# Optimization experiments

Hardware: AMD Instinct MI355X
Metric: run time of the kernel (lower is better)

Reference implementation:

```python
import jax, jax.numpy as jnp
import numpy as np

T, H, I, E, K = 2048, 1024, 768, 32, 4  # tokens, hidden, expert intermediate, n_experts, top_k


def setup_inputs() -> dict:
    key = jax.random.key(0)
    k0, k1, k2, k3, k4 = jax.random.split(key, 5)
    scale = 0.02
    return {
        "x": jax.random.normal(k0, (T, H), dtype=jnp.float32),
        "gate_w": jax.random.normal(k1, (E, H), dtype=jnp.float32) * scale,   # router linear [E, H]
        "w_gate": jax.random.normal(k2, (E, I, H), dtype=jnp.float32) * scale,  # gate_proj per expert
        "w_up": jax.random.normal(k3, (E, I, H), dtype=jnp.float32) * scale,    # up_proj per expert
        "w_down": jax.random.normal(k4, (E, H, I), dtype=jnp.float32) * scale,  # down_proj per expert
    }


def reference(x, gate_w, w_gate, w_up, w_down):
    # Router: dense gate linear + softmax + top-k + renormalize
    logits = x @ gate_w.T                              # [T, E]
    probs = jax.nn.softmax(logits, axis=-1)
    top_w, top_i = jax.lax.top_k(probs, K)             # [T, K]
    top_w = top_w / jnp.sum(top_w, axis=-1, keepdims=True)  # renormalize=True
    # Dense combine weights [T, E] (zero for unselected experts)
    tok = jnp.arange(T, dtype=jnp.int32)[:, None]
    combine = jnp.zeros((T, E), dtype=x.dtype).at[tok, top_i].add(top_w)

    # Scan over experts: each expert is a SwiGLU MLP; masked-dense combine.
    def step(acc, ws):
        w1, w3, w2, ce = ws                            # [I,H], [I,H], [H,I], [T]
        h = (jax.nn.silu(x @ w1.T) * (x @ w3.T)) @ w2.T  # [T, H]
        return acc + ce[:, None] * h, None

    out, _ = jax.lax.scan(step, jnp.zeros_like(x), (w_gate, w_up, w_down, combine.T))
    return out
```

## Files before the change

kernel.cpp:

```cpp
#include <hip/hip_runtime.h>
#include <hip/hip_bf16.h>
#include <stdint.h>

#define T_TOK 2048
#define HDIM  1024
#define IDIM  768
#define NEXP  32
#define TOPK  4
#define NPAIR (T_TOK*TOPK)
#define MTILE 384
#define MAXMT 64

typedef __attribute__((ext_vector_type(8))) short bf16x8;
typedef __attribute__((ext_vector_type(4))) float f32x4;

#define SBAR0() __builtin_amdgcn_sched_barrier(0)
#define LBAR()  do{ asm volatile("s_waitcnt lgkmcnt(0)" ::: "memory"); \
                    __builtin_amdgcn_s_barrier(); SBAR0(); }while(0)

__device__ __forceinline__ unsigned short f2bf(float f){
  union { float f; unsigned u; } v; v.f = f;
  unsigned r = (v.u + 0x7fffu + ((v.u >> 16) & 1u)) >> 16;
  return (unsigned short)r;
}

__device__ __forceinline__ unsigned pack_bf2(float lo, float hi){
  __hip_bfloat162 h2 = __float22bfloat162_rn(float2{lo, hi});
  union { __hip_bfloat162 h; unsigned u; } v; v.h = h2;
  return v.u;
}

__global__ __launch_bounds__(256) void k_convert_x(const float* __restrict__ x,
                                                   ushort* __restrict__ xb){
  int idx = blockIdx.x*256 + threadIdx.x;
  float4 v = ((const float4*)x)[idx];
  ushort4 o; o.x=f2bf(v.x); o.y=f2bf(v.y); o.z=f2bf(v.z); o.w=f2bf(v.w);
  ((ushort4*)xb)[idx] = o;
}

__global__ __launch_bounds__(256) void k_router(const float* __restrict__ x,
                                                const float* __restrict__ gw,
                                                int* __restrict__ ei, float* __restrict__ wv,
                                                int* __restrict__ counts){
  int wid  = threadIdx.x >> 6;
  int lane = threadIdx.x & 63;
  int t = blockIdx.x*4 + wid;
  float xv[16];
  #pragma unroll
  for (int i=0;i<16;i++) xv[i] = x[t*HDIM + i*64 + lane];
  float p[NEXP];
  #pragma unroll
  for (int e=0;e<NEXP;e++){
    const float* w = gw + e*HDIM;
    float a = 0.f;
    #pragma unroll
    for (int i=0;i<16;i++) a = fmaf(xv[i], w[i*64+lane], a);
    #pragma unroll
    for (int off=32; off>=1; off>>=1) a += __shfl_xor(a, off, 64);
    p[e] = a;
  }
  float m = p[0];
  #pragma unroll
  for (int e=1;e<NEXP;e++) m = fmaxf(m, p[e]);
  #pragma unroll
  for (int e=0;e<NEXP;e++) p[e] = __expf(p[e]-m);
  unsigned used = 0; int sel[TOPK]; float sw[TOPK]; float wsum = 0.f;
  #pragma unroll
  for (int k=0;k<TOPK;k++){
    float best = -1.f; int bi = 0;
    #pragma unroll
    for (int e=0;e<NEXP;e++){
      bool ok = (((used>>e)&1u)==0u) && (p[e] > best);
      best = ok ? p[e] : best; bi = ok ? e : bi;
    }
    used |= 1u<<bi; sel[k]=bi; sw[k]=best; wsum += best;
  }
  if (lane==0){
    float inv = 1.f/wsum;
    #pragma unroll
    for (int k=0;k<TOPK;k++){
      ei[t*TOPK+k] = sel[k];
      wv[t*TOPK+k] = sw[k]*inv;
      atomicAdd(&counts[sel[k]], 1);
    }
  }
}

__global__ void k_offsets(const int* __restrict__ counts, int* __restrict__ offsets,
                          int* __restrict__ mtE, int* __restrict__ mtM0,
                          int* __restrict__ nmt){
  if (threadIdx.x==0 && blockIdx.x==0){
    int s=0;
    for (int e=0;e<NEXP;e++){ offsets[e]=s; s+=counts[e]; }
    offsets[NEXP]=s;
    int nm=0;
    for (int e=0;e<NEXP;e++){
      int ne = counts[e];
      for (int m0=0; m0<ne && nm<MAXMT; m0+=MTILE){ mtE[nm]=e; mtM0[nm]=m0; nm++; }
    }
    nmt[0]=nm;
  }
}

__global__ __launch_bounds__(256) void k_scatter(const int* __restrict__ ei,
                                                 const int* __restrict__ offsets,
                                                 int* __restrict__ cursor,
                                                 int* __restrict__ slot_tk,
                                                 int* __restrict__ tk_slot){
  int g = blockIdx.x*256 + threadIdx.x;
  int e = ei[g];
  int pos = atomicAdd(&cursor[e], 1);
  int slot = offsets[e] + pos;
  slot_tk[slot] = g;
  tk_slot[g] = slot;
}

__global__ __launch_bounds__(512,3) void k_gateup(const ushort* __restrict__ xb,
    const float* __restrict__ w1, const float* __restrict__ w3,
    const int* __restrict__ offsets, const int* __restrict__ slot_tk,
    const int* __restrict__ mtE, const int* __restrict__ mtM0, const int* __restrict__ nmt,
    ushort* __restrict__ act){
  const int NH = 8;
  int bi  = blockIdx.x;
  int xcd = bi & 7, j = bi >> 3;
  int mti = (j/24)*8 + xcd;
  int it  = j % 24;
  if (mti >= nmt[0]) return;
  int e    = mtE[mti];
  int m0   = mtM0[mti];
  int off0 = offsets[e];
  int ne   = offsets[e+1]-off0;
  int ibase = it*32;

  __shared__ ushort Bls[2][64][136];
  __shared__ int toks[MTILE];

  int tid = threadIdx.x, wid = tid>>6, lane = tid&63;
  if (tid < MTILE){
    int slot = off0 + m0 + tid;
    int fb = slot_tk[off0] >> 2;
    toks[tid] = (m0 + tid < ne) ? (slot_tk[slot] >> 2) : fb;
  }
  __syncthreads();

  const float* bp[4]; int brow_s[4];
  #pragma unroll
  for (int s=0;s<4;s++){
    int row = s*16 + wid*2 + (lane>>5);
    brow_s[s] = row;
    int mat = row>>5, ir = row&31;
    bp[s] = (mat ? w3 : w1) + (size_t)e*IDIM*HDIM
          + (size_t)(ibase+ir)*HDIM + (lane&31)*4;
  }
  int q = lane>>4;
  const ushort* arow[3];
  #pragma unroll
  for (int m=0;m<3;m++){
    int row = wid*48 + m*16 + (lane&15);
    arow[m] = xb + (size_t)toks[row]*HDIM + q*8;
  }

  f32x4 accg[3][2], accu[3][2];
  #pragma unroll
  for (int m=0;m<3;m++)
    #pragma unroll
    for (int n=0;n<2;n++){ accg[m][n]=(f32x4){0,0,0,0}; accu[m][n]=(f32x4){0,0,0,0}; }

  float4 breg[4];
  bf16x8 aA[3][4];

  auto loadB = [&](int t){
    #pragma unroll
    for (int s=0;s<4;s++) breg[s] = *(const float4*)(bp[s] + t*128);
  };
  auto writeB = [&](int buf){
    #pragma unroll
    for (int s=0;s<4;s++){
      uint2 u; u.x = pack_bf2(breg[s].x, breg[s].y); u.y = pack_bf2(breg[s].z, breg[s].w);
      *(uint2*)(&Bls[buf][brow_s[s]][(lane&31)*4]) = u;
    }
  };
  auto loadA = [&](int t){
    #pragma unroll
    for (int m=0;m<3;m++)
      #pragma unroll
      for (int kk=0;kk<4;kk++)
        aA[m][kk] = *(const bf16x8*)(arow[m] + t*128 + kk*32);
  };
  auto compute = [&](int buf){
    #pragma unroll
    for (int kk=0;kk<4;kk++){
      #pragma unroll
      for (int nf=0;nf<2;nf++){
        bf16x8 bg = *(const bf16x8*)(&Bls[buf][     nf*16 + (lane&15)][kk*32 + q*8]);
        bf16x8 bu = *(const bf16x8*)(&Bls[buf][32 + nf*16 + (lane&15)][kk*32 + q*8]);
        #pragma unroll
        for (int m=0;m<3;m++){
          accg[m][nf] = __builtin_amdgcn_mfma_f32_16x16x32_bf16(aA[m][kk], bg, accg[m][nf], 0,0,0);
          accu[m][nf] = __builtin_amdgcn_mfma_f32_16x16x32_bf16(aA[m][kk], bu, accu[m][nf], 0,0,0);
        }
      }
    }
  };

  loadB(0);
  writeB(0);
  loadA(0);
  SBAR0();
  loadB(1);
  LBAR();

  #pragma unroll 2
  for (int h=0; h<NH; ++h){
    compute(h&1);
    if (h+1 < NH){
      writeB((h+1)&1);
      loadA(h+1);
      SBAR0();
      if (h+2 < NH) loadB(h+2);
      LBAR();
    }
  }

  int nval = ne - m0; if (nval > MTILE) nval = MTILE;
  #pragma unroll
  for (int m=0;m<3;m++)
    #pragma unroll
    for (int nf=0;nf<2;nf++)
      #pragma unroll
      for (int r=0;r<4;r++){
        int row = wid*48 + m*16 + (lane>>4)*4 + r;
        if (row < nval){
          float g = accg[m][nf][r], u = accu[m][nf][r];
          float sval = g / (1.f + __expf(-g)) * u;
          act[(size_t)(off0+m0+row)*IDIM + ibase + nf*16 + (lane&15)] = f2bf(sval);
        }
      }
}

__global__ __launch_bounds__(512,3) void k_down(const ushort* __restrict__ act,
    const float* __restrict__ w2, const int* __restrict__ offsets,
    const int* __restrict__ mtE, const int* __restrict__ mtM0, const int* __restrict__ nmt,
    float* __restrict__ pout){
  const int NH = 6;
  int bi  = blockIdx.x;
  int xcd = bi & 7, j = bi >> 3;
  int mti = (j>>4)*8 + xcd;
  int ht  = j & 15;
  if (mti >= nmt[0]) return;
  int e    = mtE[mti];
  int m0   = mtM0[mti];
  int off0 = offsets[e], ne = offsets[e+1]-off0;
  int hbase = ht*64;

  __shared__ ushort Bls[2][64][136];

  int tid = threadIdx.x, wid = tid>>6, lane = tid&63;

  const float* bp[4]; int brow_s[4];
  #pragma unroll
  for (int s=0;s<4;s++){
    int row = s*16 + wid*2 + (lane>>5);
    brow_s[s] = row;
    bp[s] = w2 + (size_t)e*HDIM*IDIM + (size_t)(hbase+row)*IDIM + (lane&31)*4;
  }
  int q = lane>>4;
  const ushort* arow[3];
  #pragma unroll
  for (int m=0;m<3;m++){
    int row = m0 + wid*48 + m*16 + (lane&15);
    row = (row < ne) ? row : (ne-1);
    arow[m] = act + (size_t)(off0+row)*IDIM + q*8;
  }

  f32x4 acc[3][4];
  #pragma unroll
  for (int m=0;m<3;m++)
    #pragma unroll
    for (int n=0;n<4;n++) acc[m][n]=(f32x4){0,0,0,0};

  float4 breg[4];
  bf16x8 aA[3][4];

  auto loadB = [&](int t){
    #pragma unroll
    for (int s=0;s<4;s++) breg[s] = *(const float4*)(bp[s] + t*128);
  };
  auto writeB = [&](int buf){
    #pragma unroll
    for (int s=0;s<4;s++){
      uint2 u; u.x = pack_bf2(breg[s].x, breg[s].y); u.y = pack_bf2(breg[s].z, breg[s].w);
      *(uint2*)(&Bls[buf][brow_s[s]][(lane&31)*4]) = u;
    }
  };
  auto loadA = [&](int t){
    #pragma unroll
    for (int m=0;m<3;m++)
      #pragma unroll
      for (int kk=0;kk<4;kk++)
        aA[m][kk] = *(const bf16x8*)(arow[m] + t*128 + kk*32);
  };
  auto compute = [&](int buf){
    #pragma unroll
    for (int kk=0;kk<4;kk++){
      #pragma unroll
      for (int nf=0;nf<4;nf++){
        bf16x8 bw = *(const bf16x8*)(&Bls[buf][nf*16 + (lane&15)][kk*32 + q*8]);
        #pragma unroll
        for (int m=0;m<3;m++)
          acc[m][nf] = __builtin_amdgcn_mfma_f32_16x16x32_bf16(aA[m][kk], bw, acc[m][nf], 0,0,0);
      }
    }
  };

  loadB(0);
  writeB(0);
  loadA(0);
  SBAR0();
  loadB(1);
  LBAR();

  #pragma unroll 2
  for (int h=0; h<NH; ++h){
    compute(h&1);
    if (h+1 < NH){
      writeB((h+1)&1);
      loadA(h+1);
      SBAR0();
      if (h+2 < NH) loadB(h+2);
      LBAR();
    }
  }

  int nval = ne - m0; if (nval > MTILE) nval = MTILE;
  #pragma unroll
  for (int m=0;m<3;m++)
    #pragma unroll
    for (int nf=0;nf<4;nf++)
      #pragma unroll
      for (int r=0;r<4;r++){
        int row = wid*48 + m*16 + (lane>>4)*4 + r;
        if (row < nval)
          pout[(size_t)(off0+m0+row)*HDIM + hbase + nf*16 + (lane&15)] = acc[m][nf][r];
      }
}

__global__ __launch_bounds__(256) void k_combine(const float* __restrict__ pout,
    const int* __restrict__ tk_slot, const float* __restrict__ wv,
    float* __restrict__ out){
  int t = blockIdx.x;
  int c = threadIdx.x;
  float a0=0,a1=0,a2=0,a3=0;
  #pragma unroll
  for (int k=0;k<TOPK;k++){
    int slot = tk_slot[t*TOPK+k];
    float w  = wv[t*TOPK+k];
    float4 v = *(const float4*)(pout + (size_t)slot*HDIM + c*4);
    a0 = fmaf(w, v.x, a0); a1 = fmaf(w, v.y, a1);
    a2 = fmaf(w, v.z, a2); a3 = fmaf(w, v.w, a3);
  }
  float4 o; o.x=a0; o.y=a1; o.z=a2; o.w=a3;
  *(float4*)(out + (size_t)t*HDIM + c*4) = o;
}

extern "C" void kernel_launch(void* const* d_in, const int* in_sizes, int n_in,
                              void* d_out, int out_size, void* d_ws, size_t ws_size,
                              hipStream_t stream){
  const float* x  = (const float*)d_in[0];
  const float* gw = (const float*)d_in[1];
  const float* w1 = (const float*)d_in[2];
  const float* w3 = (const float*)d_in[3];
  const float* w2 = (const float*)d_in[4];
  float* out = (float*)d_out;

  char* ws = (char*)d_ws;
  size_t off = 0;
  ushort* xb   = (ushort*)(ws + off); off += (size_t)T_TOK*HDIM*2;
  ushort* act  = (ushort*)(ws + off); off += (size_t)NPAIR*IDIM*2;
  float*  pout = (float*) (ws + off); off += (size_t)NPAIR*HDIM*4;
  int* counts  = (int*)(ws + off); off += NEXP*4;
  int* cursor  = (int*)(ws + off); off += NEXP*4;
  int* offsets = (int*)(ws + off); off += (NEXP+1)*4;
  int* mtE     = (int*)(ws + off); off += MAXMT*4;
  int* mtM0    = (int*)(ws + off); off += MAXMT*4;
  int* nmt     = (int*)(ws + off); off += 4;
  off = (off + 255) & ~(size_t)255;
  int*   ei      = (int*)  (ws + off); off += (size_t)NPAIR*4;
  float* wvp     = (float*)(ws + off); off += (size_t)NPAIR*4;
  int*   slot_tk = (int*)  (ws + off); off += (size_t)NPAIR*4;
  int*   tk_slot = (int*)  (ws + off); off += (size_t)NPAIR*4;

  hipMemsetAsync(counts, 0, 2*NEXP*4, stream);

  k_convert_x<<<T_TOK*HDIM/1024, 256, 0, stream>>>(x, xb);
  k_router<<<T_TOK/4, 256, 0, stream>>>(x, gw, ei, wvp, counts);
  k_offsets<<<1, 64, 0, stream>>>(counts, offsets, mtE, mtM0, nmt);
  k_scatter<<<NPAIR/256, 256, 0, stream>>>(ei, offsets, cursor, slot_tk, tk_slot);
  k_gateup<<<1536, 512, 0, stream>>>(xb, w1, w3, offsets, slot_tk, mtE, mtM0, nmt, act);
  k_down<<<1024, 512, 0, stream>>>(act, w2, offsets, mtE, mtM0, nmt, pout);
  k_combine<<<T_TOK, 256, 0, stream>>>(pout, tk_slot, wvp, out);
}
```

Before: 238.0 us.

## Triple-buffer GEMM K-loop with smaller K-steps and fuse x conversion into router

The gate/up and down GEMM kernels move from a double-buffered 128-wide K step to a triple-buffered 64-wide K step. Weights are prefetched three stages ahead in registers and the loop is fully unrolled, and launch bounds rise to allow four blocks per CU. Separately, the fp32-to-bf16 conversion of x is folded into the router kernel, which removes one kernel launch and one extra read pass over x. The trade-off is more barriers per unit of work and higher register pressure under the tighter occupancy bound.

New measurement: 223.2 us. -6.2%, faster.

```diff
diff --git a/kernel.cpp b/kernel.cpp
--- a/kernel.cpp
+++ b/kernel.cpp
@@ -30,18 +30,11 @@
   return v.u;
 }
 
-__global__ __launch_bounds__(256) void k_convert_x(const float* __restrict__ x,
-                                                   ushort* __restrict__ xb){
-  int idx = blockIdx.x*256 + threadIdx.x;
-  float4 v = ((const float4*)x)[idx];
-  ushort4 o; o.x=f2bf(v.x); o.y=f2bf(v.y); o.z=f2bf(v.z); o.w=f2bf(v.w);
-  ((ushort4*)xb)[idx] = o;
-}
-
 __global__ __launch_bounds__(256) void k_router(const float* __restrict__ x,
                                                 const float* __restrict__ gw,
                                                 int* __restrict__ ei, float* __restrict__ wv,
-                                                int* __restrict__ counts){
+                                                int* __restrict__ counts,
+                                                ushort* __restrict__ xb){
   int wid  = threadIdx.x >> 6;
   int lane = threadIdx.x & 63;
   int t = blockIdx.x*4 + wid;
@@ -83,6 +76,12 @@
       wv[t*TOPK+k] = sw[k]*inv;
       atomicAdd(&counts[sel[k]], 1);
     }
+  }
+  #pragma unroll
+  for (int kq=0;kq<4;kq++){
+    float4 v = *(const float4*)(x + (size_t)t*HDIM + (kq*64+lane)*4);
+    ushort4 o; o.x=f2bf(v.x); o.y=f2bf(v.y); o.z=f2bf(v.z); o.w=f2bf(v.w);
+    *(ushort4*)(xb + (size_t)t*HDIM + (kq*64+lane)*4) = o;
   }
 }
 
@@ -115,16 +114,16 @@
   tk_slot[g] = slot;
 }
 
-__global__ __launch_bounds__(512,3) void k_gateup(const ushort* __restrict__ xb,
+__global__ __launch_bounds__(512,4) void k_gateup(const ushort* __restrict__ xb,
     const float* __restrict__ w1, const float* __restrict__ w3,
     const int* __restrict__ offsets, const int* __restrict__ slot_tk,
     const int* __restrict__ mtE, const int* __restrict__ mtM0, const int* __restrict__ nmt,
     ushort* __restrict__ act){
-  const int NH = 8;
+  const int NHS = 16;
   int bi  = blockIdx.x;
-  int xcd = bi & 7, j = bi >> 3;
-  int mti = (j/24)*8 + xcd;
-  int it  = j % 24;
+  int s   = bi >> 3;
+  int mti = (s/24)*8 + (bi&7);
+  int it  = s % 24;
   if (mti >= nmt[0]) return;
   int e    = mtE[mti];
   int m0   = mtM0[mti];
@@ -132,7 +131,7 @@
   int ne   = offsets[e+1]-off0;
   int ibase = it*32;
 
-  __shared__ ushort Bls[2][64][136];
+  __shared__ ushort Bls[3][64][72];
   __shared__ int toks[MTILE];
 
   int tid = threadIdx.x, wid = tid>>6, lane = tid&63;
@@ -143,14 +142,14 @@
   }
   __syncthreads();
 
-  const float* bp[4]; int brow_s[4];
-  #pragma unroll
-  for (int s=0;s<4;s++){
-    int row = s*16 + wid*2 + (lane>>5);
-    brow_s[s] = row;
+  const float* bp[2]; int brow_s[2];
+  #pragma unroll
+  for (int ss=0;ss<2;ss++){
+    int row = ss*32 + wid*4 + (lane>>4);
+    brow_s[ss] = row;
     int mat = row>>5, ir = row&31;
-    bp[s] = (mat ? w3 : w1) + (size_t)e*IDIM*HDIM
-          + (size_t)(ibase+ir)*HDIM + (lane&31)*4;
+    bp[ss] = (mat ? w3 : w1) + (size_t)e*IDIM*HDIM
+           + (size_t)(ibase+ir)*HDIM + (lane&15)*4;
   }
   int q = lane>>4;
   const ushort* arow[3];
@@ -166,30 +165,30 @@
     #pragma unroll
     for (int n=0;n<2;n++){ accg[m][n]=(f32x4){0,0,0,0}; accu[m][n]=(f32x4){0,0,0,0}; }
 
-  float4 breg[4];
-  bf16x8 aA[3][4];
-
-  auto loadB = [&](int t){
-    #pragma unroll
-    for (int s=0;s<4;s++) breg[s] = *(const float4*)(bp[s] + t*128);
-  };
-  auto writeB = [&](int buf){
-    #pragma unroll
-    for (int s=0;s<4;s++){
-      uint2 u; u.x = pack_bf2(breg[s].x, breg[s].y); u.y = pack_bf2(breg[s].z, breg[s].w);
-      *(uint2*)(&Bls[buf][brow_s[s]][(lane&31)*4]) = u;
+  float4 b0[2], b1[2], b2[2];
+  bf16x8 aA[3][2];
+
+  auto loadB = [&](int t, float4 (&d)[2]){
+    d[0] = *(const float4*)(bp[0] + t*64);
+    d[1] = *(const float4*)(bp[1] + t*64);
+  };
+  auto writeB = [&](int buf, const float4 (&sv)[2]){
+    #pragma unroll
+    for (int ss=0;ss<2;ss++){
+      uint2 u; u.x = pack_bf2(sv[ss].x, sv[ss].y); u.y = pack_bf2(sv[ss].z, sv[ss].w);
+      *(uint2*)(&Bls[buf][brow_s[ss]][(lane&15)*4]) = u;
     }
   };
   auto loadA = [&](int t){
     #pragma unroll
     for (int m=0;m<3;m++)
       #pragma unroll
-      for (int kk=0;kk<4;kk++)
-        aA[m][kk] = *(const bf16x8*)(arow[m] + t*128 + kk*32);
-  };
-  auto compute = [&](int buf){
-    #pragma unroll
-    for (int kk=0;kk<4;kk++){
+      for (int kk=0;kk<2;kk++)
+        aA[m][kk] = *(const bf16x8*)(arow[m] + t*64 + kk*32);
+  };
+  auto computeK = [&](int buf){
+    #pragma unroll
+    for (int kk=0;kk<2;kk++){
       #pragma unroll
       for (int nf=0;nf<2;nf++){
         bf16x8 bg = *(const bf16x8*)(&Bls[buf][     nf*16 + (lane&15)][kk*32 + q*8]);
@@ -203,24 +202,27 @@
     }
   };
 
-  loadB(0);
-  writeB(0);
+  loadB(0, b0);
   loadA(0);
-  SBAR0();
-  loadB(1);
+  loadB(1, b1);
+  writeB(0, b0);
+  loadB(2, b2);
   LBAR();
 
-  #pragma unroll 2
-  for (int h=0; h<NH; ++h){
-    compute(h&1);
-    if (h+1 < NH){
-      writeB((h+1)&1);
-      loadA(h+1);
-      SBAR0();
-      if (h+2 < NH) loadB(h+2);
-      LBAR();
-    }
-  }
+#define GUSTEP(h, cb, wb, BW, BL) \
+  computeK(cb); \
+  if ((h)+1 < NHS) loadA((h)+1); \
+  if ((h)+3 < NHS) loadB((h)+3, BL); \
+  if ((h)+1 < NHS) writeB(wb, BW); \
+  LBAR();
+
+  GUSTEP(0, 0, 1, b1, b0)  GUSTEP(1, 1, 2, b2, b1)  GUSTEP(2, 2, 0, b0, b2)
+  GUSTEP(3, 0, 1, b1, b0)  GUSTEP(4, 1, 2, b2, b1)  GUSTEP(5, 2, 0, b0, b2)
+  GUSTEP(6, 0, 1, b1, b0)  GUSTEP(7, 1, 2, b2, b1)  GUSTEP(8, 2, 0, b0, b2)
+  GUSTEP(9, 0, 1, b1, b0)  GUSTEP(10,1, 2, b2, b1)  GUSTEP(11,2, 0, b0, b2)
+  GUSTEP(12,0, 1, b1, b0)  GUSTEP(13,1, 2, b2, b1)  GUSTEP(14,2, 0, b0, b2)
+  GUSTEP(15,0, 1, b1, b0)
+#undef GUSTEP
 
   int nval = ne - m0; if (nval > MTILE) nval = MTILE;
   #pragma unroll
@@ -238,31 +240,31 @@
       }
 }
 
-__global__ __launch_bounds__(512,3) void k_down(const ushort* __restrict__ act,
+__global__ __launch_bounds__(512,4) void k_down(const ushort* __restrict__ act,
     const float* __restrict__ w2, const int* __restrict__ offsets,
     const int* __restrict__ mtE, const int* __restrict__ mtM0, const int* __restrict__ nmt,
     float* __restrict__ pout){
-  const int NH = 6;
+  const int NHS = 12;
   int bi  = blockIdx.x;
-  int xcd = bi & 7, j = bi >> 3;
-  int mti = (j>>4)*8 + xcd;
-  int ht  = j & 15;
+  int s   = bi >> 3;
+  int mti = (s>>4)*8 + (bi&7);
+  int ht  = s & 15;
   if (mti >= nmt[0]) return;
   int e    = mtE[mti];
   int m0   = mtM0[mti];
   int off0 = offsets[e], ne = offsets[e+1]-off0;
   int hbase = ht*64;
 
-  __shared__ ushort Bls[2][64][136];
+  __shared__ ushort Bls[3][64][72];
 
   int tid = threadIdx.x, wid = tid>>6, lane = tid&63;
 
-  const float* bp[4]; int brow_s[4];
-  #pragma unroll
-  for (int s=0;s<4;s++){
-    int row = s*16 + wid*2 + (lane>>5);
-    brow_s[s] = row;
-    bp[s] = w2 + (size_t)e*HDIM*IDIM + (size_t)(hbase+row)*IDIM + (lane&31)*4;
+  const float* bp[2]; int brow_s[2];
+  #pragma unroll
+  for (int ss=0;ss<2;ss++){
+    int row = ss*32 + wid*4 + (lane>>4);
+    brow_s[ss] = row;
+    bp[ss] = w2 + (size_t)e*HDIM*IDIM + (size_t)(hbase+row)*IDIM + (lane&15)*4;
   }
   int q = lane>>4;
   const ushort* arow[3];
@@ -279,30 +281,30 @@
     #pragma unroll
     for (int n=0;n<4;n++) acc[m][n]=(f32x4){0,0,0,0};
 
-  float4 breg[4];
-  bf16x8 aA[3][4];
-
-  auto loadB = [&](int t){
-    #pragma unroll
-    for (int s=0;s<4;s++) breg[s] = *(const float4*)(bp[s] + t*128);
-  };
-  auto writeB = [&](int buf){
-    #pragma unroll
-    for (int s=0;s<4;s++){
-      uint2 u; u.x = pack_bf2(breg[s].x, breg[s].y); u.y = pack_bf2(breg[s].z, breg[s].w);
-      *(uint2*)(&Bls[buf][brow_s[s]][(lane&31)*4]) = u;
+  float4 b0[2], b1[2], b2[2];
+  bf16x8 aA[3][2];
+
+  auto loadB = [&](int t, float4 (&d)[2]){
+    d[0] = *(const float4*)(bp[0] + t*64);
+    d[1] = *(const float4*)(bp[1] + t*64);
+  };
+  auto writeB = [&](int buf, const float4 (&sv)[2]){
+    #pragma unroll
+    for (int ss=0;ss<2;ss++){
+      uint2 u; u.x = pack_bf2(sv[ss].x, sv[ss].y); u.y = pack_bf2(sv[ss].z, sv[ss].w);
+      *(uint2*)(&Bls[buf][brow_s[ss]][(lane&15)*4]) = u;
     }
   };
   auto loadA = [&](int t){
     #pragma unroll
     for (int m=0;m<3;m++)
       #pragma unroll
-      for (int kk=0;kk<4;kk++)
-        aA[m][kk] = *(const bf16x8*)(arow[m] + t*128 + kk*32);
-  };
-  auto compute = [&](int buf){
-    #pragma unroll
-    for (int kk=0;kk<4;kk++){
+      for (int kk=0;kk<2;kk++)
+        aA[m][kk] = *(const bf16x8*)(arow[m] + t*64 + kk*32);
+  };
+  auto computeK = [&](int buf){
+    #pragma unroll
+    for (int kk=0;kk<2;kk++){
       #pragma unroll
       for (int nf=0;nf<4;nf++){
         bf16x8 bw = *(const bf16x8*)(&Bls[buf][nf*16 + (lane&15)][kk*32 + q*8]);
@@ -313,24 +315,25 @@
     }
   };
 
-  loadB(0);
-  writeB(0);
+  loadB(0, b0);
   loadA(0);
-  SBAR0();
-  loadB(1);
+  loadB(1, b1);
+  writeB(0, b0);
+  loadB(2, b2);
   LBAR();
 
-  #pragma unroll 2
-  for (int h=0; h<NH; ++h){
-    compute(h&1);
-    if (h+1 < NH){
-      writeB((h+1)&1);
-      loadA(h+1);
-      SBAR0();
-      if (h+2 < NH) loadB(h+2);
-      LBAR();
-    }
-  }
+#define DNSTEP(h, cb, wb, BW, BL) \
+  computeK(cb); \
+  if ((h)+1 < NHS) loadA((h)+1); \
+  if ((h)+3 < NHS) loadB((h)+3, BL); \
+  if ((h)+1 < NHS) writeB(wb, BW); \
+  LBAR();
+
+  DNSTEP(0, 0, 1, b1, b0)  DNSTEP(1, 1, 2, b2, b1)  DNSTEP(2, 2, 0, b0, b2)
+  DNSTEP(3, 0, 1, b1, b0)  DNSTEP(4, 1, 2, b2, b1)  DNSTEP(5, 2, 0, b0, b2)
+  DNSTEP(6, 0, 1, b1, b0)  DNSTEP(7, 1, 2, b2, b1)  DNSTEP(8, 2, 0, b0, b2)
+  DNSTEP(9, 0, 1, b1, b0)  DNSTEP(10,1, 2, b2, b1)  DNSTEP(11,2, 0, b0, b2)
+#undef DNSTEP
 
   int nval = ne - m0; if (nval > MTILE) nval = MTILE;
   #pragma unroll
@@ -392,8 +395,7 @@
 
   hipMemsetAsync(counts, 0, 2*NEXP*4, stream);
 
-  k_convert_x<<<T_TOK*HDIM/1024, 256, 0, stream>>>(x, xb);
-  k_router<<<T_TOK/4, 256, 0, stream>>>(x, gw, ei, wvp, counts);
+  k_router<<<T_TOK/4, 256, 0, stream>>>(x, gw, ei, wvp, counts, xb);
   k_offsets<<<1, 64, 0, stream>>>(counts, offsets, mtE, mtM0, nmt);
   k_scatter<<<NPAIR/256, 256, 0, stream>>>(ei, offsets, cursor, slot_tk, tk_slot);
   k_gateup<<<1536, 512, 0, stream>>>(xb, w1, w3, offsets, slot_tk, mtE, mtM0, nmt, act);
```
